# Optimization experiments

Hardware: AMD Instinct MI355X
Metric: run time of the kernel (lower is better)

The kernel has to match this reference:

```python
import jax, jax.numpy as jnp
import numpy as np


def _conv1d(x, W, b):
    # x: [B, Cin, L], W: [Cout, Cin, K], SAME padding (odd K)
    pad = (W.shape[-1] - 1) // 2
    y = jax.lax.conv_general_dilated(
        x, W, window_strides=(1,), padding=[(pad, pad)],
        dimension_numbers=('NCH', 'OIH', 'NCH'))
    return y + b[None, :, None]


def _conv_lstm_layer(x_tm, W, b, h0, c0):
    # x_tm: [T, B, Cin, L]; returns stacked hidden states [T, B, F, L]
    def step(carry, x_t):
        h, c = carry
        A = _conv1d(jnp.concatenate([x_t, h], axis=1), W, b)  # [B, 4F, L]
        ai, af, ao, ag = jnp.split(A, 4, axis=1)
        next_c = jax.nn.sigmoid(af) * c + jax.nn.sigmoid(ai) * jnp.tanh(ag)
        next_h = jax.nn.sigmoid(ao) * jnp.tanh(next_c)
        return (next_h, next_c), next_h
    (_, _), hs = jax.lax.scan(step, (h0, c0), x_tm)
    return hs


def setup_inputs() -> dict:
    key = jax.random.key(0)
    ks = jax.random.split(key, 5)
    B, T, Cin, L, F, K = 8, 64, 64, 256, 128, 5
    x = jax.random.normal(ks[0], (B, T, Cin, L), dtype=jnp.float32)
    W0 = jax.random.normal(ks[1], (4 * F, Cin + F, K), dtype=jnp.float32) * 0.05
    b0 = jax.random.normal(ks[2], (4 * F,), dtype=jnp.float32) * 0.05
    W1 = jax.random.normal(ks[3], (4 * F, F + F, K), dtype=jnp.float32) * 0.05
    b1 = jax.random.normal(ks[4], (4 * F,), dtype=jnp.float32) * 0.05
    z = jnp.zeros((B, F, L), dtype=jnp.float32)
    return {"x": x, "W0": W0, "b0": b0, "W1": W1, "b1": b1,
            "h0": z, "c0": z, "h1": z, "c1": z}


def reference(x, W0, b0, W1, b1, h0, c0, h1, c1):
    # x: [B, T, C, L] -> time-major [T, B, C, L] as in torch transpose(0,1)
    x_tm = jnp.transpose(x, (1, 0, 2, 3))
    hs0 = _conv_lstm_layer(x_tm, W0, b0, h0, c0)   # [T, B, F, L]
    hs1 = _conv_lstm_layer(hs0, W1, b1, h1, c1)    # [T, B, F, L]
    return hs1
```

## Files before the change

### kernel.cpp

```cpp
#include <hip/hip_runtime.h>
#include <math.h>

#define B_SZ 8
#define T_SZ 64
#define CIN 64
#define L_LEN 256
#define F_CH 128
#define K_W 5
#define S_BFL (B_SZ * F_CH * L_LEN)

typedef short bf16x8 __attribute__((ext_vector_type(8)));
typedef float f32x4  __attribute__((ext_vector_type(4)));
typedef unsigned int  uint_t;
typedef unsigned short ushort_t;

__device__ __forceinline__ float sigmoid_f(float x) {
    return 1.0f / (1.0f + __expf(-x));
}
__device__ __forceinline__ float tanh_f(float x) {
    float a = fabsf(x);
    float e = __expf(-2.0f * a);
    float t = (1.0f - e) / (1.0f + e);
    return copysignf(t, x);
}
__device__ __forceinline__ ushort_t bf16rne(float f) {
    uint_t u = __float_as_uint(f);
    uint_t r = (u + 0x7FFFu + ((u >> 16) & 1u)) >> 16;
    return (ushort_t)r;
}
__device__ __forceinline__ uint_t pack_f32(float v) {
    ushort_t h = bf16rne(v);
    float hf = __uint_as_float(((uint_t)h) << 16);
    ushort_t l = bf16rne(v - hf);
    return (uint_t)h | (((uint_t)l) << 16);
}

union FragU { uint4 q; bf16x8 v; f32x4 f; float4 f4; };

template<int CTOT>
__global__ __launch_bounds__(256)
void convert_w(const float* __restrict__ W, ushort_t* __restrict__ Ahi,
               ushort_t* __restrict__ Alo)
{
    constexpr int KS = CTOT / 32;
    const int idx = blockIdx.x * 256 + threadIdx.x;
    if (idx >= 5 * KS * 4 * 512) return;
    const int r    = idx & 511;
    int rest       = idx >> 9;
    const int koct = rest & 3;  rest >>= 2;
    const int ks   = rest % KS;
    const int tap  = rest / KS;
    const int f = r >> 2, g = r & 3;
    const int row = g * F_CH + f;
    #pragma unroll
    for (int j = 0; j < 8; ++j) {
        int c = ks * 32 + koct * 8 + j;
        float w = W[(row * CTOT + c) * K_W + tap];
        ushort_t h = bf16rne(w);
        ushort_t l = bf16rne(w - __uint_as_float(((uint_t)h) << 16));
        Ahi[idx * 8 + j] = h;
        Alo[idx * 8 + j] = l;
    }
}

__global__ __launch_bounds__(256)
void remap_bias(const float* __restrict__ b0, const float* __restrict__ b1,
                float* __restrict__ br0, float* __restrict__ br1)
{
    int r = blockIdx.x * 256 + threadIdx.x;
    if (r < 512)       br0[r] = b0[(r & 3) * F_CH + (r >> 2)];
    else { r -= 512;   br1[r] = b1[(r & 3) * F_CH + (r >> 2)]; }
}

__global__ __launch_bounds__(256)
void ws_init(const float* __restrict__ h0, const float* __restrict__ h1,
             const float* __restrict__ c0, const float* __restrict__ c1,
             uint_t* __restrict__ hp0a, uint_t* __restrict__ hp0b,
             uint_t* __restrict__ hp1a, uint_t* __restrict__ hp1b,
             float* __restrict__ c0w, float* __restrict__ c1w)
{
    int i = blockIdx.x * 256 + threadIdx.x;
    if (i < S_BFL) {
        uint_t p0 = pack_f32(h0[i]);
        uint_t p1 = pack_f32(h1[i]);
        hp0a[i] = p0; hp0b[i] = p0;
        hp1a[i] = p1; hp1b[i] = p1;
        c0w[i] = c0[i];
        c1w[i] = c1[i];
    }
}

template<int C0, int CTOT, bool IN0_F32>
__device__ void step_body(uint_t* __restrict__ sh, const int tid,
    const int mblk, const int b, const int l0,
    const float* __restrict__ in0f, int in0_b_stride,
    const uint_t* __restrict__ in0p,
    const uint_t* __restrict__ hprevp,
    const ushort_t* __restrict__ Ahi, const ushort_t* __restrict__ Alo,
    const float* __restrict__ biasr,
    const float* __restrict__ c_in, float* __restrict__ c_out,
    float* __restrict__ h_out_f32,
    uint_t* __restrict__ hp_out)
{
    constexpr int KS = CTOT / 32;
    constexpr int KK = 5 * KS;
    constexpr int STRIDE = CTOT + 4;
    constexpr int LP = 132;

    constexpr int TOT = LP * CTOT;
    constexpr int U = (TOT + 1023) / 1024;
    #pragma unroll
    for (int r = 0; r < 2; ++r) {
        uint_t v[U];
        #pragma unroll
        for (int u = 0; u < U; ++u) {
            const int i = r * (512 * U) + u * 512 + tid;
            if (i < TOT) {
                const int c  = i / LP, lp = i - c * LP;
                const int gl = l0 + lp - 2;
                const int glc = min(max(gl, 0), L_LEN - 1);
                if (IN0_F32) {
                    const float* s = (c < C0) ? (in0f + b * in0_b_stride + c * L_LEN)
                                              : nullptr;
                    v[u] = (c < C0) ? __float_as_uint(s[glc])
                                    : hprevp[(b * F_CH + (c - C0)) * L_LEN + glc];
                } else {
                    v[u] = (c < C0) ? in0p[(b * C0 + c) * L_LEN + glc]
                                    : hprevp[(b * F_CH + (c - C0)) * L_LEN + glc];
                }
            }
        }
        #pragma unroll
        for (int u = 0; u < U; ++u) {
            const int i = r * (512 * U) + u * 512 + tid;
            if (i < TOT) {
                const int c  = i / LP, lp = i - c * LP;
                const int gl = l0 + lp - 2;
                uint_t w = v[u];
                if (IN0_F32 && c < C0) w = pack_f32(__uint_as_float(w));
                if (gl < 0 || gl >= L_LEN) w = 0u;
                sh[lp * STRIDE + c] = w;
            }
        }
    }
    __syncthreads();

    const int w_id = tid >> 6;
    const int q    = w_id & 3;
    const int nh   = w_id >> 2;
    const int lane = tid & 63;
    const int l16  = lane & 15, oct = lane >> 4;
    const int mrow = mblk * 64 + l16;
    const int k_lo = (q * KK) / 4, k_hi = ((q + 1) * KK) / 4;

    f32x4 acc[4][4];
    #pragma unroll
    for (int mt = 0; mt < 4; ++mt)
        #pragma unroll
        for (int nf = 0; nf < 4; ++nf) acc[mt][nf] = (f32x4)0.0f;

    const uint4* AH4 = (const uint4*)Ahi;
    const uint4* AL4 = (const uint4*)Alo;
    const uint4* shq = (const uint4*)sh;

    uint4 A0[8], A1[8];
    auto loadA = [&](int kk, uint4* dst) {
        const int base = (kk * 4 + oct) * 512 + mrow;
        #pragma unroll
        for (int mt = 0; mt < 4; ++mt) {
            dst[2 * mt]     = AH4[base + 16 * mt];
            dst[2 * mt + 1] = AL4[base + 16 * mt];
        }
    };
    auto body = [&](int kk, uint4* A) {
        const int tap = kk / KS, ks = kk - tap * KS;
        const int cb  = ks * 8 + oct * 2;
        bf16x8 bh[4], bl[4];
        #pragma unroll
        for (int nf = 0; nf < 4; ++nf) {
            const int row = nh * 64 + nf * 16 + l16 + tap;
            const int r = row * (STRIDE / 4) + cb;
            uint4 p0 = shq[r], p1 = shq[r + 1];
            FragU H, L;
            H.q.x = __builtin_amdgcn_perm(p0.y, p0.x, 0x05040100u);
            H.q.y = __builtin_amdgcn_perm(p0.w, p0.z, 0x05040100u);
            H.q.z = __builtin_amdgcn_perm(p1.y, p1.x, 0x05040100u);
            H.q.w = __builtin_amdgcn_perm(p1.w, p1.z, 0x05040100u);
            L.q.x = __builtin_amdgcn_perm(p0.y, p0.x, 0x07060302u);
            L.q.y = __builtin_amdgcn_perm(p0.w, p0.z, 0x07060302u);
            L.q.z = __builtin_amdgcn_perm(p1.y, p1.x, 0x07060302u);
            L.q.w = __builtin_amdgcn_perm(p1.w, p1.z, 0x07060302u);
            bh[nf] = H.v; bl[nf] = L.v;
        }
        #pragma unroll
        for (int mt = 0; mt < 4; ++mt) {
            FragU TH, TL; TH.q = A[2 * mt]; TL.q = A[2 * mt + 1];
            bf16x8 ah = TH.v, al = TL.v;
            #pragma unroll
            for (int nf = 0; nf < 4; ++nf) {
                acc[mt][nf] = __builtin_amdgcn_mfma_f32_16x16x32_bf16(ah, bh[nf], acc[mt][nf], 0, 0, 0);
                acc[mt][nf] = __builtin_amdgcn_mfma_f32_16x16x32_bf16(al, bh[nf], acc[mt][nf], 0, 0, 0);
                acc[mt][nf] = __builtin_amdgcn_mfma_f32_16x16x32_bf16(ah, bl[nf], acc[mt][nf], 0, 0, 0);
            }
        }
    };

    loadA(k_lo, A0);
    for (int kk = k_lo; kk < k_hi; kk += 2) {
        loadA(kk + 1 < k_hi ? kk + 1 : kk, A1);
        body(kk, A0);
        loadA(kk + 2 < k_hi ? kk + 2 : kk, A0);
        if (kk + 1 < k_hi) body(kk + 1, A1);
    }

    __syncthreads();
    float4* scratch = (float4*)sh;
    #pragma unroll
    for (int mt = 0; mt < 4; ++mt)
        #pragma unroll
        for (int nf = 0; nf < 4; ++nf) {
            FragU u; u.f = acc[mt][nf];
            scratch[(w_id * 16 + mt * 4 + nf) * 64 + lane] = u.f4;
        }
    __syncthreads();

    #pragma unroll
    for (int nf = 0; nf < 4; ++nf) {
        float4 s = scratch[((nh * 4 + 0) * 16 + q * 4 + nf) * 64 + lane];
        #pragma unroll
        for (int w = 1; w < 4; ++w) {
            float4 p = scratch[((nh * 4 + w) * 16 + q * 4 + nf) * 64 + lane];
            s.x += p.x; s.y += p.y; s.z += p.z; s.w += p.w;
        }
        const int rbase = mblk * 64 + q * 16 + 4 * oct;
        const float4 b4 = *(const float4*)(biasr + rbase);
        const int f = rbase >> 2;
        float gi = sigmoid_f(s.x + b4.x);
        float gf = sigmoid_f(s.y + b4.y);
        float go = sigmoid_f(s.z + b4.z);
        float gg = tanh_f(s.w + b4.w);
        const int l   = l0 + nh * 64 + nf * 16 + l16;
        const int idx = (b * F_CH + f) * L_LEN + l;
        float cp = c_in[idx];
        float cn = gf * cp + gi * gg;
        float hn = go * tanh_f(cn);
        c_out[idx] = cn;
        if (h_out_f32) h_out_f32[idx] = hn;
        hp_out[idx] = pack_f32(hn);
    }
}

struct FusedParams {
    const float* x;
    const ushort_t* Ahi0; const ushort_t* Alo0;
    const ushort_t* Ahi1; const ushort_t* Alo1;
    const float* br0; const float* br1;
    float* c0w; float* c1w;
    uint_t* hp0a; uint_t* hp0b;
    uint_t* hp1a; uint_t* hp1b;
    float* out;
};

__global__ __launch_bounds__(512, 2)
void fused_step(FusedParams P, int t)
{
    constexpr int SH_WORDS = 132 * (256 + 4);
    __shared__ __align__(16) uint_t sh[SH_WORDS];

    const int tid  = threadIdx.x;
    const int bx   = blockIdx.x;
    const int mblk = bx & 7;
    const int nblk = (bx & 127) >> 3;
    const int b    = nblk >> 1;
    const int l0   = (nblk & 1) << 7;

    if (bx < 128) {
        if (t >= 1) {
            const int tt = t - 1;
            const uint_t* hp0cur  = (tt & 1) ? P.hp0b : P.hp0a;
            const uint_t* hp1prev = (tt & 1) ? P.hp1a : P.hp1b;
            uint_t*       hp1w    = (tt & 1) ? P.hp1b : P.hp1a;
            step_body<F_CH, 256, false>(sh, tid, mblk, b, l0,
                (const float*)nullptr, 0, hp0cur,
                hp1prev, P.Ahi1, P.Alo1, P.br1,
                P.c1w, P.c1w,
                P.out + (size_t)tt * S_BFL, hp1w);
        }
    } else {
        if (t < T_SZ) {
            const uint_t* hp0prev = (t & 1) ? P.hp0a : P.hp0b;
            uint_t*       hp0w    = (t & 1) ? P.hp0b : P.hp0a;
            step_body<CIN, 192, true>(sh, tid, mblk, b, l0,
                P.x + (size_t)t * CIN * L_LEN, T_SZ * CIN * L_LEN,
                (const uint_t*)nullptr,
                hp0prev, P.Ahi0, P.Alo0, P.br0,
                P.c0w, P.c0w,
                (float*)nullptr, hp0w);
        }
    }
}

extern "C" void kernel_launch(void* const* d_in, const int* in_sizes, int n_in,
                              void* d_out, int out_size, void* d_ws, size_t ws_size,
                              hipStream_t stream)
{
    const float* x  = (const float*)d_in[0];
    const float* W0 = (const float*)d_in[1];
    const float* b0 = (const float*)d_in[2];
    const float* W1 = (const float*)d_in[3];
    const float* b1 = (const float*)d_in[4];
    const float* h0 = (const float*)d_in[5];
    const float* c0 = (const float*)d_in[6];
    const float* h1 = (const float*)d_in[7];
    const float* c1 = (const float*)d_in[8];
    float* out = (float*)d_out;

    const int S = S_BFL;
    float* ws  = (float*)d_ws;
    float* c0w = ws;
    float* c1w = ws + S;
    float* br0 = ws + 2 * S;
    float* br1 = br0 + 512;
    uint_t* hp0a = (uint_t*)(ws + 2 * S + 1024);
    uint_t* hp0b = hp0a + S;
    uint_t* hp1a = hp0b + S;
    uint_t* hp1b = hp1a + S;
    ushort_t* Ahi0 = (ushort_t*)(hp1b + S);
    const int N0 = 512 * 192 * 5;
    const int N1 = 512 * 256 * 5;
    ushort_t* Alo0 = Ahi0 + N0;
    ushort_t* Ahi1 = Alo0 + N0;
    ushort_t* Alo1 = Ahi1 + N1;

    convert_w<192><<<dim3(240), dim3(256), 0, stream>>>(W0, Ahi0, Alo0);
    convert_w<256><<<dim3(320), dim3(256), 0, stream>>>(W1, Ahi1, Alo1);
    remap_bias<<<dim3(4), dim3(256), 0, stream>>>(b0, b1, br0, br1);
    ws_init<<<dim3((S + 255) / 256), dim3(256), 0, stream>>>(
        h0, h1, c0, c1, hp0a, hp0b, hp1a, hp1b, c0w, c1w);

    FusedParams P;
    P.x = x;
    P.Ahi0 = Ahi0; P.Alo0 = Alo0; P.Ahi1 = Ahi1; P.Alo1 = Alo1;
    P.br0 = br0; P.br1 = br1;
    P.c0w = c0w; P.c1w = c1w;
    P.hp0a = hp0a; P.hp0b = hp0b; P.hp1a = hp1a; P.hp1b = hp1b;
    P.out = out;

    dim3 grid(256), block(512);
    for (int t = 0; t <= T_SZ; ++t) {
        fused_step<<<grid, block, 0, stream>>>(P, t);
    }
}
```

Before: 1.428 ms.

## Merge prepass kernels, triple-buffer weight fragment loads, relax launch bounds

```diff
diff --git a/kernel.cpp b/kernel.cpp
--- a/kernel.cpp
+++ b/kernel.cpp
@@ -38,12 +38,11 @@
 union FragU { uint4 q; bf16x8 v; f32x4 f; float4 f4; };
 
 template<int CTOT>
-__global__ __launch_bounds__(256)
-void convert_w(const float* __restrict__ W, ushort_t* __restrict__ Ahi,
-               ushort_t* __restrict__ Alo)
+__device__ void convert_w_body(int idx, const float* __restrict__ W,
+                               ushort_t* __restrict__ Ahi,
+                               ushort_t* __restrict__ Alo)
 {
     constexpr int KS = CTOT / 32;
-    const int idx = blockIdx.x * 256 + threadIdx.x;
     if (idx >= 5 * KS * 4 * 512) return;
     const int r    = idx & 511;
     int rest       = idx >> 9;
@@ -64,29 +63,36 @@
 }
 
 __global__ __launch_bounds__(256)
-void remap_bias(const float* __restrict__ b0, const float* __restrict__ b1,
-                float* __restrict__ br0, float* __restrict__ br1)
-{
-    int r = blockIdx.x * 256 + threadIdx.x;
-    if (r < 512)       br0[r] = b0[(r & 3) * F_CH + (r >> 2)];
-    else { r -= 512;   br1[r] = b1[(r & 3) * F_CH + (r >> 2)]; }
-}
-
-__global__ __launch_bounds__(256)
-void ws_init(const float* __restrict__ h0, const float* __restrict__ h1,
+void prepass(const float* __restrict__ W0, const float* __restrict__ W1,
+             const float* __restrict__ b0, const float* __restrict__ b1,
+             const float* __restrict__ h0, const float* __restrict__ h1,
              const float* __restrict__ c0, const float* __restrict__ c1,
+             ushort_t* __restrict__ Ahi0, ushort_t* __restrict__ Alo0,
+             ushort_t* __restrict__ Ahi1, ushort_t* __restrict__ Alo1,
+             float* __restrict__ br0, float* __restrict__ br1,
              uint_t* __restrict__ hp0a, uint_t* __restrict__ hp0b,
              uint_t* __restrict__ hp1a, uint_t* __restrict__ hp1b,
              float* __restrict__ c0w, float* __restrict__ c1w)
 {
-    int i = blockIdx.x * 256 + threadIdx.x;
-    if (i < S_BFL) {
-        uint_t p0 = pack_f32(h0[i]);
-        uint_t p1 = pack_f32(h1[i]);
-        hp0a[i] = p0; hp0b[i] = p0;
-        hp1a[i] = p1; hp1b[i] = p1;
-        c0w[i] = c0[i];
-        c1w[i] = c1[i];
+    const int bx = blockIdx.x;
+    if (bx < 240) {
+        convert_w_body<192>(bx * 256 + threadIdx.x, W0, Ahi0, Alo0);
+    } else if (bx < 560) {
+        convert_w_body<256>((bx - 240) * 256 + threadIdx.x, W1, Ahi1, Alo1);
+    } else if (bx < 564) {
+        int r = (bx - 560) * 256 + threadIdx.x;
+        if (r < 512)       br0[r] = b0[(r & 3) * F_CH + (r >> 2)];
+        else { r -= 512;   br1[r] = b1[(r & 3) * F_CH + (r >> 2)]; }
+    } else {
+        int i = (bx - 564) * 256 + threadIdx.x;
+        if (i < S_BFL) {
+            uint_t p0 = pack_f32(h0[i]);
+            uint_t p1 = pack_f32(h1[i]);
+            hp0a[i] = p0; hp0b[i] = p0;
+            hp1a[i] = p1; hp1b[i] = p1;
+            c0w[i] = c0[i];
+            c1w[i] = c1[i];
+        }
     }
 }
 
@@ -163,8 +169,9 @@
     const uint4* AL4 = (const uint4*)Alo;
     const uint4* shq = (const uint4*)sh;
 
-    uint4 A0[8], A1[8];
+    uint4 A0[8], A1[8], A2[8];
     auto loadA = [&](int kk, uint4* dst) {
+        kk = min(kk, k_hi - 1);
         const int base = (kk * 4 + oct) * 512 + mrow;
         #pragma unroll
         for (int mt = 0; mt < 4; ++mt) {
@@ -206,12 +213,15 @@
     };
 
     loadA(k_lo, A0);
-    for (int kk = k_lo; kk < k_hi; kk += 2) {
-        loadA(kk + 1 < k_hi ? kk + 1 : kk, A1);
-        body(kk, A0);
-        loadA(kk + 2 < k_hi ? kk + 2 : kk, A0);
-        if (kk + 1 < k_hi) body(kk + 1, A1);
-    }
+    loadA(k_lo + 1, A1);
+    int kk = k_lo;
+    for (; kk + 3 <= k_hi; kk += 3) {
+        loadA(kk + 2, A2); body(kk,     A0);
+        loadA(kk + 3, A0); body(kk + 1, A1);
+        loadA(kk + 4, A1); body(kk + 2, A2);
+    }
+    if (kk     < k_hi) body(kk,     A0);
+    if (kk + 1 < k_hi) body(kk + 1, A1);
 
     __syncthreads();
     float4* scratch = (float4*)sh;
@@ -261,7 +271,7 @@
     float* out;
 };
 
-__global__ __launch_bounds__(512, 2)
+__global__ __launch_bounds__(512)
 void fused_step(FusedParams P, int t)
 {
     constexpr int SH_WORDS = 132 * (256 + 4);
@@ -332,11 +342,10 @@
     ushort_t* Ahi1 = Alo0 + N0;
     ushort_t* Alo1 = Ahi1 + N1;
 
-    convert_w<192><<<dim3(240), dim3(256), 0, stream>>>(W0, Ahi0, Alo0);
-    convert_w<256><<<dim3(320), dim3(256), 0, stream>>>(W1, Ahi1, Alo1);
-    remap_bias<<<dim3(4), dim3(256), 0, stream>>>(b0, b1, br0, br1);
-    ws_init<<<dim3((S + 255) / 256), dim3(256), 0, stream>>>(
-        h0, h1, c0, c1, hp0a, hp0b, hp1a, hp1b, c0w, c1w);
+    prepass<<<dim3(240 + 320 + 4 + 1024), dim3(256), 0, stream>>>(
+        W0, W1, b0, b1, h0, h1, c0, c1,
+        Ahi0, Alo0, Ahi1, Alo1, br0, br1,
+        hp0a, hp0b, hp1a, hp1b, c0w, c1w);
 
     FusedParams P;
     P.x = x;
```

Result: faster. 1.376 ms (-3.6%).
